# Kernel tuning notes

Measured on AMD Instinct MI355X. Metric: run time of the kernel, lower is better.

Reference implementation:

```python
import jax, jax.numpy as jnp
import numpy as np

S, N, V, E, H, L = 40, 256, 32000, 1024, 1024, 2


def _gru_step(x, h, wih, whh, bih, bhh):
    # PyTorch GRU cell, gate order [r, z, n]
    gi = x @ wih.T + bih          # (N, 3H)
    gh = h @ whh.T + bhh          # (N, 3H)
    ir, iz, inn = jnp.split(gi, 3, axis=-1)
    hr, hz, hn = jnp.split(gh, 3, axis=-1)
    r = jax.nn.sigmoid(ir + hr)
    z = jax.nn.sigmoid(iz + hz)
    n = jnp.tanh(inn + r * hn)
    return (1.0 - z) * n + z * h


def setup_inputs() -> dict:
    key = jax.random.key(0)
    ks = jax.random.split(key, 16)
    nrm = lambda k, shp: (jax.random.normal(k, shp, jnp.float32) * 0.05)
    return {
        "tokens": jax.random.randint(ks[0], (S, N), 0, V),
        "hidden": jnp.zeros((L, N, H), jnp.float32),
        "emb": nrm(ks[1], (V, E)),
        "enc_wih": nrm(ks[2], (L, 3 * H, E)),
        "enc_whh": nrm(ks[3], (L, 3 * H, H)),
        "enc_bih": nrm(ks[4], (L, 3 * H)),
        "enc_bhh": nrm(ks[5], (L, 3 * H)),
        "dec_wih": nrm(ks[6], (L, 3 * H, H)),
        "dec_whh": nrm(ks[7], (L, 3 * H, H)),
        "dec_bih": nrm(ks[8], (L, 3 * H)),
        "dec_bhh": nrm(ks[9], (L, 3 * H)),
        "attn_w": nrm(ks[10], (S, E + L * H)),
        "attn_b": nrm(ks[11], (S,)),
        "comb_w": nrm(ks[12], (H, 2 * H)),
        "comb_b": nrm(ks[13], (H,)),
    }


def reference(tokens, hidden, emb, enc_wih, enc_whh, enc_bih, enc_bhh,
              dec_wih, dec_whh, dec_bih, dec_bhh,
              attn_w, attn_b, comb_w, comb_b):
    x = emb[tokens]                      # (S, N, E) embedded input

    # ---- encoder: 2-layer GRU over the full sequence ----
    seq = x
    h_finals = []
    for l in range(L):
        wih, whh, bih, bhh = enc_wih[l], enc_whh[l], enc_bih[l], enc_bhh[l]
        def step(h, xt, wih=wih, whh=whh, bih=bih, bhh=bhh):
            h2 = _gru_step(xt, h, wih, whh, bih, bhh)
            return h2, h2
        hT, seq = jax.lax.scan(step, hidden[l], seq)
        h_finals.append(hT)
    h_n = jnp.stack(h_finals)            # (L, N, H)
    enc_out = jnp.swapaxes(seq, 0, 1)    # (N, S, H)

    # ---- attention decoder: scan over timesteps, carry decoder hidden ----
    def dec_step(h, emb_t):
        # h: (L, N, H), emb_t: (N, E)
        h_flat = jnp.swapaxes(h, 0, 1).reshape(N, L * H)
        logits = jnp.concatenate([emb_t, h_flat], axis=-1) @ attn_w.T + attn_b
        aw = jax.nn.softmax(logits, axis=-1)                   # (N, S)
        applied = jnp.einsum('ns,nsh->nh', aw, enc_out)        # (N, H)
        xcur = jax.nn.relu(
            jnp.concatenate([emb_t, applied], axis=-1) @ comb_w.T + comb_b)
        hs = []
        for l in range(L):
            hl = _gru_step(xcur, h[l], dec_wih[l], dec_whh[l],
                           dec_bih[l], dec_bhh[l])
            hs.append(hl)
            xcur = hl
        return jnp.stack(hs), xcur

    hT, outs = jax.lax.scan(dec_step, h_n, x)   # outs: (S, N, H)
    return outs, hT
```

## Files before the change

### kernel.cpp

```cpp
#include <hip/hip_runtime.h>
#include <hip/hip_bf16.h>

#define S_LEN 40
#define NB    256
#define EDIM  1024
#define HDIM  1024
#define NBLK  256
#define NTHR  768

typedef _Float16 f16;
typedef __attribute__((ext_vector_type(8))) _Float16 f16x8;
typedef __attribute__((ext_vector_type(4))) _Float16 f16x4;
typedef __attribute__((ext_vector_type(4))) float f32x4;

__device__ __forceinline__ float sigm(float x) {
    x = fminf(fmaxf(x, -30.f), 30.f);
    return 1.f / (1.f + __expf(-x));
}
__device__ __forceinline__ float tanh_fast(float x) {
    x = fminf(fmaxf(x, -15.f), 15.f);
    float e = __expf(2.f * x);
    return (e - 1.f) / (e + 1.f);
}

__device__ __forceinline__ void sysst_f16(f16* p, f16 v) {
    union { f16 f; unsigned short s; } u; u.f = v;
    unsigned int b = u.s;
    asm volatile("global_store_short %0, %1, off sc0 sc1" :: "v"(p), "v"(b) : "memory");
}

__device__ __forceinline__ void gbar1(unsigned* cnt, unsigned* gen) {
    asm volatile("s_waitcnt vmcnt(0)" ::: "memory");
    __syncthreads();
    if (threadIdx.x == 0) {
        unsigned g = __hip_atomic_load(gen, __ATOMIC_RELAXED, __HIP_MEMORY_SCOPE_AGENT);
        unsigned a = __hip_atomic_fetch_add(cnt, 1u, __ATOMIC_RELEASE, __HIP_MEMORY_SCOPE_AGENT);
        if (a == NBLK - 1) {
            __hip_atomic_store(cnt, 0u, __ATOMIC_RELAXED, __HIP_MEMORY_SCOPE_AGENT);
            __hip_atomic_fetch_add(gen, 1u, __ATOMIC_RELEASE, __HIP_MEMORY_SCOPE_AGENT);
        } else {
            while (__hip_atomic_load(gen, __ATOMIC_RELAXED, __HIP_MEMORY_SCOPE_AGENT) == g)
                __builtin_amdgcn_s_sleep(2);
        }
    }
    __syncthreads();
}

__device__ __forceinline__ void g2bar(unsigned* sync, unsigned xcd,
                                      unsigned M, unsigned NX) {
    asm volatile("s_waitcnt vmcnt(0)" ::: "memory");
    __syncthreads();
    if (threadIdx.x == 0) {
        unsigned* ggen = sync;
        unsigned* gcnt = sync + 1;
        unsigned* xa = sync + 16 + xcd * 16;
        unsigned g = __hip_atomic_load(ggen, __ATOMIC_RELAXED, __HIP_MEMORY_SCOPE_AGENT);
        unsigned a = __hip_atomic_fetch_add(xa, 1u, __ATOMIC_RELEASE, __HIP_MEMORY_SCOPE_AGENT);
        if (a == M - 1) {
            __hip_atomic_store(xa, 0u, __ATOMIC_RELAXED, __HIP_MEMORY_SCOPE_AGENT);
            unsigned b = __hip_atomic_fetch_add(gcnt, 1u, __ATOMIC_RELEASE, __HIP_MEMORY_SCOPE_AGENT);
            if (b == NX - 1) {
                __hip_atomic_store(gcnt, 0u, __ATOMIC_RELAXED, __HIP_MEMORY_SCOPE_AGENT);
                __hip_atomic_fetch_add(ggen, 1u, __ATOMIC_RELEASE, __HIP_MEMORY_SCOPE_AGENT);
            } else {
                while (__hip_atomic_load(ggen, __ATOMIC_RELAXED, __HIP_MEMORY_SCOPE_AGENT) == g)
                    __builtin_amdgcn_s_sleep(4);
            }
        } else {
            while (__hip_atomic_load(ggen, __ATOMIC_RELAXED, __HIP_MEMORY_SCOPE_AGENT) == g)
                __builtin_amdgcn_s_sleep(4);
        }
    }
    __syncthreads();
}

__global__ void k_init_sync(unsigned* s) {
    for (int k = threadIdx.x; k < 1024; k += 256) s[k] = 0;
}

__device__ __forceinline__ void probe_mn(int lane, int* mrow, int* ncol) {
    f16x8 pa, pb;
#pragma unroll
    for (int e = 0; e < 8; e++) {
        pa[e] = (f16)(float)(lane & 15);
        pb[e] = (f16)0.03125f;
    }
    f32x4 pacc = {0, 0, 0, 0};
    pacc = __builtin_amdgcn_mfma_f32_16x16x32_f16(pa, pb, pacc, 0, 0, 0);
#pragma unroll
    for (int r = 0; r < 4; r++) {
        int m = (int)(pacc[r] + 0.5f);
        int cg = ((lane >> 4) << 2) + r;
        mrow[r] = m;
        ncol[r] = (m == cg) ? (lane & 15) : cg;
    }
}

__global__ __launch_bounds__(256) void k_cvt4(const float* __restrict__ src,
                                              f16* __restrict__ dst, int n4) {
    int i = blockIdx.x * 256 + threadIdx.x;
    if (i < n4) {
        f32x4 v = ((const f32x4*)src)[i];
        f16x4 o = {(f16)v.x, (f16)v.y, (f16)v.z, (f16)v.w};
        ((f16x4*)dst)[i] = o;
    }
}
__global__ __launch_bounds__(256) void k_embed_cvt(const int* __restrict__ tok,
                                                   const float* __restrict__ emb,
                                                   f16* __restrict__ xe) {
    int b = blockIdx.x;
    int t = threadIdx.x;
    int token = tok[b];
    f32x4 v = ((const f32x4*)(emb + (size_t)token * EDIM))[t];
    f16x4 o = {(f16)v.x, (f16)v.y, (f16)v.z, (f16)v.w};
    ((f16x4*)(xe + (size_t)b * EDIM))[t] = o;
}

__device__ void gru_phase(
    char* lds, int cb, int rb, int tid, const int* mr, const int* nc,
    const f16* __restrict__ xsrc, const f16* __restrict__ hsrc,
    const f16* __restrict__ wih, const f16* __restrict__ whh,
    const float* __restrict__ bih, const float* __restrict__ bhh,
    f16* ho16, float* of_step, float* of_fin) {

    {
        constexpr int TOT = 8192;
        constexpr int IT = (TOT + NTHR - 1) / NTHR;
        f16x8 val[IT];
#pragma unroll
        for (int i = 0; i < IT; i++) {
            int c = tid + i * NTHR;
            if (c < TOT) {
                int isH = c >> 12;
                int cl = c & 4095;
                int row = cl >> 7, cc = cl & 127;
                const f16* src = (isH ? hsrc : xsrc) +
                                 (size_t)(rb + row) * 1024 + cc * 8;
                val[i] = *(const f16x8*)src;
            }
        }
#pragma unroll
        for (int i = 0; i < IT; i++) {
            int c = tid + i * NTHR;
            if (c < TOT) {
                int isH = c >> 12;
                int cl = c & 4095;
                int row = cl >> 7, cc = cl & 127;
                *(f16x8*)(lds + isH * 65536 + row * 2048 +
                          ((cc ^ (row & 7)) << 4)) = val[i];
            }
        }
    }
    __syncthreads();

    const int w = tid >> 6, lane = tid & 63;
    const int pair = w >> 1, kh = w & 1;
    const int gate = (pair >= 3) ? pair - 3 : pair;
    const int r0 = lane & 15, kk0 = (lane >> 4) * 8;
    const f16* B = ((pair < 3) ? wih : whh) + ((size_t)gate * HDIM + cb) * 1024;
    const f16* B0 = B + (size_t)r0 * 1024 + kk0 + kh * 512;
    const f16* B1 = B + (size_t)(r0 + 16) * 1024 + kk0 + kh * 512;
    const int abase = (pair < 3) ? 0 : 65536;
    const int swz = r0 & 7;
    const char* a0p = lds + abase + r0 * 2048;
    const char* a1p = lds + abase + (r0 + 16) * 2048;

    f32x4 acc00 = {0,0,0,0}, acc01 = {0,0,0,0}, acc10 = {0,0,0,0}, acc11 = {0,0,0,0};
#pragma unroll 4
    for (int k = 0; k < 512; k += 32) {
        int g = (kh * 512 + kk0 + k) >> 3;
        int off = (g ^ swz) << 4;
        f16x8 a0 = *(const f16x8*)(a0p + off);
        f16x8 a1 = *(const f16x8*)(a1p + off);
        f16x8 b0 = *(const f16x8*)(B0 + k);
        f16x8 b1 = *(const f16x8*)(B1 + k);
        acc00 = __builtin_amdgcn_mfma_f32_16x16x32_f16(a0, b0, acc00, 0, 0, 0);
        acc01 = __builtin_amdgcn_mfma_f32_16x16x32_f16(a0, b1, acc01, 0, 0, 0);
        acc10 = __builtin_amdgcn_mfma_f32_16x16x32_f16(a1, b0, acc10, 0, 0, 0);
        acc11 = __builtin_amdgcn_mfma_f32_16x16x32_f16(a1, b1, acc11, 0, 0, 0);
    }
    __syncthreads();

    float* red = (float*)lds;
    float* rw = red + w * 1024;
#pragma unroll
    for (int r = 0; r < 4; r++) {
        rw[mr[r] * 32 + nc[r]]             = acc00[r];
        rw[mr[r] * 32 + nc[r] + 16]        = acc01[r];
        rw[(mr[r] + 16) * 32 + nc[r]]      = acc10[r];
        rw[(mr[r] + 16) * 32 + nc[r] + 16] = acc11[r];
    }
    __syncthreads();

#pragma unroll
    for (int it = 0; it < 2; it++) {
        int i = tid + it * NTHR;
        if (i < 1024) {
            int rr = i >> 5, ccn = i & 31;
            int col = cb + ccn;
            int row = rb + rr;
            float gir = red[i]         + red[1024 + i];
            float giz = red[2048 + i]  + red[3072 + i];
            float gin = red[4096 + i]  + red[5120 + i];
            float ghr = red[6144 + i]  + red[7168 + i];
            float ghz = red[8192 + i]  + red[9216 + i];
            float ghn = red[10240 + i] + red[11264 + i];
            float r = sigm(gir + bih[col] + ghr + bhh[col]);
            float z = sigm(giz + bih[HDIM + col] + ghz + bhh[HDIM + col]);
            float n = tanh_fast(gin + bih[2 * HDIM + col] +
                                r * (ghn + bhh[2 * HDIM + col]));
            int gidx = col >> 3, within = col & 7;
            float hp = (float)*(const f16*)(lds + 65536 + rr * 2048 +
                                            ((gidx ^ (rr & 7)) << 4) + within * 2);
            float hn2 = (1.f - z) * n + z * hp;
            size_t idx = (size_t)row * HDIM + col;
            sysst_f16(ho16 + idx, (f16)hn2);
            if (of_step) of_step[idx] = hn2;
            if (of_fin)  of_fin[idx] = hn2;
        }
    }
}

__device__ void attn_phase(
    char* lds, int bid, int tid,
    const f16* __restrict__ xe_t, const f16* __restrict__ h0,
    const f16* __restrict__ h1,
    const f16* __restrict__ attn_w, const float* __restrict__ attn_b,
    const f16* __restrict__ enc16, f16* __restrict__ appl) {
    float* logit = (float*)(lds + 131072);
    float* awls  = logit + 64;
    const int n = bid;
    const int w = tid >> 6, lane = tid & 63;
    const size_t nrow = (size_t)n * 1024;

    {
        constexpr int TOT = 5504;
        constexpr int IT = (TOT + NTHR - 1) / NTHR;
        f16x8 val[IT];
#pragma unroll
        for (int i = 0; i < IT; i++) {
            int c = tid + i * NTHR;
            if (c < TOT) {
                if (c < 5120) {
                    int s = c >> 7, cc = c & 127;
                    val[i] = *(const f16x8*)(enc16 + ((size_t)s * NB + n) * 1024 + cc * 8);
                } else {
                    int r = c - 5120;
                    const f16* src = (r < 128) ? (xe_t + nrow + r * 8)
                                   : (r < 256) ? (h0 + nrow + (r - 128) * 8)
                                               : (h1 + nrow + (r - 256) * 8);
                    val[i] = *(const f16x8*)src;
                }
            }
        }
#pragma unroll
        for (int i = 0; i < IT; i++) {
            int c = tid + i * NTHR;
            if (c < TOT) {
                if (c < 5120) *(f16x8*)(lds + c * 16) = val[i];
                else          *(f16x8*)(lds + 81920 + (c - 5120) * 16) = val[i];
            }
        }
    }
    __syncthreads();

    if (w < 10) {
#pragma unroll
        for (int si = 0; si < 4; si++) {
            int s = w * 4 + si;
            const f16* wrow = attn_w + (size_t)s * 3072;
            float acc = 0.f;
#pragma unroll
            for (int jj = 0; jj < 6; jj++) {
                int j = lane + jj * 64;
                f16x8 a = *(const f16x8*)(lds + 81920 + j * 16);
                f16x8 b = *(const f16x8*)(wrow + j * 8);
#pragma unroll
                for (int e = 0; e < 8; e++)
                    acc = fmaf((float)a[e], (float)b[e], acc);
            }
            for (int o = 32; o; o >>= 1) acc += __shfl_down(acc, o);
            if (lane == 0) logit[s] = acc + attn_b[s];
        }
    }
    __syncthreads();

    if (w == 0) {
        float v = (lane < S_LEN) ? logit[lane] : -1e30f;
        float m = v;
        for (int o = 32; o; o >>= 1) m = fmaxf(m, __shfl_xor(m, o));
        float e = (lane < S_LEN) ? __expf(v - m) : 0.f;
        float sum = e;
        for (int o = 32; o; o >>= 1) sum += __shfl_xor(sum, o);
        if (lane < S_LEN) awls[lane] = e / sum;
    }
    __syncthreads();

    for (int col = tid; col < 1024; col += NTHR) {
        float acc = 0.f;
#pragma unroll
        for (int s = 0; s < S_LEN; s++)
            acc = fmaf(awls[s], (float)*(const f16*)(lds + s * 2048 + col * 2), acc);
        sysst_f16(appl + (size_t)n * 1024 + col, (f16)acc);
    }
}

__device__ void comb_phase(
    char* lds, int cb, int rb, int tid, const int* mr, const int* nc,
    const f16* __restrict__ xe_t, const f16* __restrict__ appl,
    const f16* __restrict__ Bw, const float* __restrict__ bias,
    f16* __restrict__ Cout) {

    {
        constexpr int TOT = 8192;
        constexpr int IT = (TOT + NTHR - 1) / NTHR;
        f16x8 val[IT];
#pragma unroll
        for (int i = 0; i < IT; i++) {
            int c = tid + i * NTHR;
            if (c < TOT) {
                int row = c >> 8, cc = c & 255;
                const f16* src = (cc < 128)
                    ? (xe_t + (size_t)(rb + row) * 1024 + cc * 8)
                    : (appl + (size_t)(rb + row) * 1024 + (cc - 128) * 8);
                val[i] = *(const f16x8*)src;
            }
        }
#pragma unroll
        for (int i = 0; i < IT; i++) {
            int c = tid + i * NTHR;
            if (c < TOT) {
                int row = c >> 8, cc = c & 255;
                *(f16x8*)(lds + row * 4096 + ((cc ^ (row & 7)) << 4)) = val[i];
            }
        }
    }
    __syncthreads();

    const int w = tid >> 6, lane = tid & 63;
    const int r0 = lane & 15, kk0 = (lane >> 4) * 8;
    const int c0 = (w * 64) / 12, c1 = ((w + 1) * 64) / 12;
    const f16* B0 = Bw + (size_t)(cb + r0) * 2048 + kk0;
    const f16* B1 = Bw + (size_t)(cb + r0 + 16) * 2048 + kk0;
    const int swz = r0 & 7;
    const char* a0p = lds + r0 * 4096;
    const char* a1p = lds + (r0 + 16) * 4096;

    f32x4 acc00 = {0,0,0,0}, acc01 = {0,0,0,0}, acc10 = {0,0,0,0}, acc11 = {0,0,0,0};
    for (int c = c0; c < c1; c++) {
        int g = (c * 32 + kk0) >> 3;
        int off = (g ^ swz) << 4;
        f16x8 a0 = *(const f16x8*)(a0p + off);
        f16x8 a1 = *(const f16x8*)(a1p + off);
        f16x8 b0 = *(const f16x8*)(B0 + c * 32);
        f16x8 b1 = *(const f16x8*)(B1 + c * 32);
        acc00 = __builtin_amdgcn_mfma_f32_16x16x32_f16(a0, b0, acc00, 0, 0, 0);
        acc01 = __builtin_amdgcn_mfma_f32_16x16x32_f16(a0, b1, acc01, 0, 0, 0);
        acc10 = __builtin_amdgcn_mfma_f32_16x16x32_f16(a1, b0, acc10, 0, 0, 0);
        acc11 = __builtin_amdgcn_mfma_f32_16x16x32_f16(a1, b1, acc11, 0, 0, 0);
    }
    __syncthreads();

    float* red = (float*)lds;
    float* rw = red + w * 1024;
#pragma unroll
    for (int r = 0; r < 4; r++) {
        rw[mr[r] * 32 + nc[r]]             = acc00[r];
        rw[mr[r] * 32 + nc[r] + 16]        = acc01[r];
        rw[(mr[r] + 16) * 32 + nc[r]]      = acc10[r];
        rw[(mr[r] + 16) * 32 + nc[r] + 16] = acc11[r];
    }
    __syncthreads();

#pragma unroll
    for (int it = 0; it < 2; it++) {
        int i = tid + it * NTHR;
        if (i < 1024) {
            float s = 0.f;
#pragma unroll
            for (int p = 0; p < 12; p++) s += red[p * 1024 + i];
            int rr = i >> 5, ccn = i & 31;
            s += bias[cb + ccn];
            s = fmaxf(s, 0.f);
            sysst_f16(Cout + (size_t)(rb + rr) * 1024 + cb + ccn, (f16)s);
        }
    }
}

__global__ __launch_bounds__(NTHR, 3) void k_mega(
    const f16* __restrict__ xe,
    f16* H0, f16* H1,
    const f16* __restrict__ w_eih, const f16* __restrict__ w_ehh,
    const float* __restrict__ enc_bih, const float* __restrict__ enc_bhh,
    const f16* __restrict__ w_dih, const f16* __restrict__ w_dhh,
    const float* __restrict__ dec_bih, const float* __restrict__ dec_bhh,
    const f16* __restrict__ w_attn, const float* __restrict__ attn_b,
    const f16* __restrict__ w_comb, const float* __restrict__ comb_b,
    f16* XC, f16* AP,
    float* out, unsigned* sync) {
    __shared__ char smem[131584];
    __shared__ unsigned s_meta[8];
    char* lds = smem;
    const int bid = blockIdx.x;
    const int tid = threadIdx.x;
    const int lane = tid & 63;
    const size_t NH = (size_t)NB * HDIM;

    int mr[4], nc[4];
    probe_mn(lane, mr, nc);

    if (tid == 0) {
        unsigned x;
        asm volatile("s_getreg_b32 %0, hwreg(20, 0, 32)" : "=s"(x));
        x &= 7;
        unsigned r = __hip_atomic_fetch_add(sync + 256 + x, 1u,
                                            __ATOMIC_RELAXED, __HIP_MEMORY_SCOPE_AGENT);
        s_meta[0] = x; s_meta[1] = r;
    }
    __syncthreads();
    gbar1(sync + 512, sync + 513);
    if (tid == 0) {
        unsigned M = __hip_atomic_load(sync + 256 + s_meta[0],
                                       __ATOMIC_RELAXED, __HIP_MEMORY_SCOPE_AGENT);
        unsigned nx = 0;
        bool uniform = true;
        for (int i = 0; i < 8; i++) {
            unsigned ci = __hip_atomic_load(sync + 256 + i, __ATOMIC_RELAXED,
                                            __HIP_MEMORY_SCOPE_AGENT);
            nx += (ci > 0) ? 1u : 0u;
            if (ci != 32) uniform = false;
        }
        s_meta[2] = M; s_meta[3] = nx;
        if (uniform) {
            s_meta[4] = (s_meta[0] * 4 + (s_meta[1] & 3)) * 32;
            s_meta[5] = (s_meta[1] >> 2) * 32;
        } else {
            s_meta[4] = (((unsigned)bid & 7) * 4 + (((unsigned)bid >> 3) & 3)) * 32;
            s_meta[5] = ((unsigned)bid >> 5) * 32;
        }
    }
    __syncthreads();
    const unsigned xcd = s_meta[0], M = s_meta[2], NX = s_meta[3];
    const int cb = (int)s_meta[4], rb = (int)s_meta[5];

    for (int t = 0; t < S_LEN; t++) {
        gru_phase(lds, cb, rb, tid, mr, nc,
                  xe + (size_t)t * NB * EDIM, H0 + (size_t)t * NH,
                  w_eih, w_ehh, enc_bih, enc_bhh,
                  H0 + (size_t)(t + 1) * NH, (float*)nullptr, (float*)nullptr);
        g2bar(sync, xcd, M, NX);
    }
    for (int t = 0; t < S_LEN; t++) {
        gru_phase(lds, cb, rb, tid, mr, nc,
                  H0 + (size_t)(t + 1) * NH, H1 + (size_t)t * NH,
                  w_eih + (size_t)3 * HDIM * EDIM, w_ehh + (size_t)3 * HDIM * HDIM,
                  enc_bih + 3 * HDIM, enc_bhh + 3 * HDIM,
                  H1 + (size_t)(t + 1) * NH, (float*)nullptr, (float*)nullptr);
        g2bar(sync, xcd, M, NX);
    }

    for (int t = 0; t < S_LEN; t++) {
        int g = S_LEN + t;
        attn_phase(lds, bid, tid,
                   xe + (size_t)t * NB * EDIM,
                   H0 + (size_t)g * NH, H1 + (size_t)g * NH,
                   w_attn, attn_b, H1 + NH, AP + (size_t)t * NH);
        g2bar(sync, xcd, M, NX);
        comb_phase(lds, cb, rb, tid, mr, nc,
                   xe + (size_t)t * NB * EDIM, AP + (size_t)t * NH,
                   w_comb, comb_b, XC + (size_t)t * NH);
        g2bar(sync, xcd, M, NX);
        gru_phase(lds, cb, rb, tid, mr, nc,
                  XC + (size_t)t * NH, H0 + (size_t)g * NH,
                  w_dih, w_dhh, dec_bih, dec_bhh,
                  H0 + (size_t)(g + 1) * NH, (float*)nullptr,
                  (t == S_LEN - 1) ? (out + (size_t)S_LEN * NH) : (float*)nullptr);
        g2bar(sync, xcd, M, NX);
        gru_phase(lds, cb, rb, tid, mr, nc,
                  H0 + (size_t)(g + 1) * NH, H1 + (size_t)g * NH,
                  w_dih + (size_t)3 * HDIM * HDIM, w_dhh + (size_t)3 * HDIM * HDIM,
                  dec_bih + 3 * HDIM, dec_bhh + 3 * HDIM,
                  H1 + (size_t)(g + 1) * NH, out + (size_t)t * NH,
                  (t == S_LEN - 1) ? (out + (size_t)(S_LEN + 1) * NH) : (float*)nullptr);
        g2bar(sync, xcd, M, NX);
    }
}

extern "C" void kernel_launch(void* const* d_in, const int* in_sizes, int n_in,
                              void* d_out, int out_size, void* d_ws, size_t ws_size,
                              hipStream_t stream) {
    const int*   tokens   = (const int*)d_in[0];
    const float* hidden   = (const float*)d_in[1];
    const float* emb      = (const float*)d_in[2];
    const float* enc_wih  = (const float*)d_in[3];
    const float* enc_whh  = (const float*)d_in[4];
    const float* enc_bih  = (const float*)d_in[5];
    const float* enc_bhh  = (const float*)d_in[6];
    const float* dec_wih  = (const float*)d_in[7];
    const float* dec_whh  = (const float*)d_in[8];
    const float* dec_bih  = (const float*)d_in[9];
    const float* dec_bhh  = (const float*)d_in[10];
    const float* attn_w   = (const float*)d_in[11];
    const float* attn_b   = (const float*)d_in[12];
    const float* comb_w   = (const float*)d_in[13];
    const float* comb_b   = (const float*)d_in[14];
    float* out = (float*)d_out;

    const size_t NH = (size_t)NB * HDIM;
    const size_t WSZ = (size_t)2 * 3 * HDIM * EDIM;

    f16* wp = (f16*)d_ws;
    f16 *w_eih = wp;  wp += WSZ;
    f16 *w_ehh = wp;  wp += WSZ;
    f16 *w_dih = wp;  wp += WSZ;
    f16 *w_dhh = wp;  wp += WSZ;
    f16 *w_comb = wp; wp += (size_t)HDIM * 2048;
    f16 *w_attn = wp; wp += (size_t)S_LEN * 3072;
    f16 *xe = wp;     wp += (size_t)S_LEN * NB * EDIM;
    f16 *H0 = wp;     wp += (size_t)(2 * S_LEN + 1) * NH;
    f16 *H1 = wp;     wp += (size_t)(2 * S_LEN + 1) * NH;
    f16 *XC = wp;     wp += (size_t)S_LEN * NH;
    f16 *AP = wp;     wp += (size_t)S_LEN * NH;
    unsigned* syncp = (unsigned*)((((uintptr_t)wp) + 255) & ~(uintptr_t)255);

    k_init_sync<<<1, 256, 0, stream>>>(syncp);

    k_cvt4<<<(int)(WSZ / 4 / 256), 256, 0, stream>>>(enc_wih, w_eih, (int)(WSZ / 4));
    k_cvt4<<<(int)(WSZ / 4 / 256), 256, 0, stream>>>(enc_whh, w_ehh, (int)(WSZ / 4));
    k_cvt4<<<(int)(WSZ / 4 / 256), 256, 0, stream>>>(dec_wih, w_dih, (int)(WSZ / 4));
    k_cvt4<<<(int)(WSZ / 4 / 256), 256, 0, stream>>>(dec_whh, w_dhh, (int)(WSZ / 4));
    k_cvt4<<<(int)(HDIM * 2048 / 4 / 256), 256, 0, stream>>>(comb_w, w_comb,
                                                             HDIM * 2048 / 4);
    k_cvt4<<<(S_LEN * 3072 / 4 + 255) / 256, 256, 0, stream>>>(attn_w, w_attn,
                                                               S_LEN * 3072 / 4);
    k_embed_cvt<<<S_LEN * NB, 256, 0, stream>>>(tokens, emb, xe);
    k_cvt4<<<(int)(NH / 4 / 256), 256, 0, stream>>>(hidden, H0, (int)(NH / 4));
    k_cvt4<<<(int)(NH / 4 / 256), 256, 0, stream>>>(hidden + NH, H1, (int)(NH / 4));

    k_mega<<<NBLK, NTHR, 0, stream>>>(
        xe, H0, H1,
        w_eih, w_ehh, enc_bih, enc_bhh,
        w_dih, w_dhh, dec_bih, dec_bhh,
        w_attn, attn_b, w_comb, comb_b,
        XC, AP, out, syncp);
}
```

Baseline: 5.441 ms.

## Read GEMM activations directly from global memory instead of staging through LDS

Removes the cooperative staging of activation tiles (x/h, comb inputs, encoder outputs) into swizzled LDS in the GRU, combine and attention phases. MFMA operands and the previous hidden value are now loaded straight from global/L2, and LDS is shrunk to just the reduction buffer and attention scratch. This cuts a staging pass and a barrier per phase and shrinks shared memory, at the cost of redundant, less coalesced global loads for the A operand. The A tile is now re-read from cache by each wave instead of once per block.

```diff
diff --git a/kernel.cpp b/kernel.cpp
--- a/kernel.cpp
+++ b/kernel.cpp
@@ -117,61 +117,29 @@
 }
 
 __device__ void gru_phase(
-    char* lds, int cb, int rb, int tid, const int* mr, const int* nc,
+    float* red, int cb, int rb, int tid, const int* mr, const int* nc,
     const f16* __restrict__ xsrc, const f16* __restrict__ hsrc,
     const f16* __restrict__ wih, const f16* __restrict__ whh,
     const float* __restrict__ bih, const float* __restrict__ bhh,
     f16* ho16, float* of_step, float* of_fin) {
 
-    {
-        constexpr int TOT = 8192;
-        constexpr int IT = (TOT + NTHR - 1) / NTHR;
-        f16x8 val[IT];
-#pragma unroll
-        for (int i = 0; i < IT; i++) {
-            int c = tid + i * NTHR;
-            if (c < TOT) {
-                int isH = c >> 12;
-                int cl = c & 4095;
-                int row = cl >> 7, cc = cl & 127;
-                const f16* src = (isH ? hsrc : xsrc) +
-                                 (size_t)(rb + row) * 1024 + cc * 8;
-                val[i] = *(const f16x8*)src;
-            }
-        }
-#pragma unroll
-        for (int i = 0; i < IT; i++) {
-            int c = tid + i * NTHR;
-            if (c < TOT) {
-                int isH = c >> 12;
-                int cl = c & 4095;
-                int row = cl >> 7, cc = cl & 127;
-                *(f16x8*)(lds + isH * 65536 + row * 2048 +
-                          ((cc ^ (row & 7)) << 4)) = val[i];
-            }
-        }
-    }
-    __syncthreads();
-
     const int w = tid >> 6, lane = tid & 63;
     const int pair = w >> 1, kh = w & 1;
     const int gate = (pair >= 3) ? pair - 3 : pair;
     const int r0 = lane & 15, kk0 = (lane >> 4) * 8;
+
+    const f16* A = (pair < 3) ? xsrc : hsrc;
+    const f16* A0 = A + (size_t)(rb + r0) * 1024 + kh * 512 + kk0;
+    const f16* A1 = A + (size_t)(rb + r0 + 16) * 1024 + kh * 512 + kk0;
     const f16* B = ((pair < 3) ? wih : whh) + ((size_t)gate * HDIM + cb) * 1024;
     const f16* B0 = B + (size_t)r0 * 1024 + kk0 + kh * 512;
     const f16* B1 = B + (size_t)(r0 + 16) * 1024 + kk0 + kh * 512;
-    const int abase = (pair < 3) ? 0 : 65536;
-    const int swz = r0 & 7;
-    const char* a0p = lds + abase + r0 * 2048;
-    const char* a1p = lds + abase + (r0 + 16) * 2048;
 
     f32x4 acc00 = {0,0,0,0}, acc01 = {0,0,0,0}, acc10 = {0,0,0,0}, acc11 = {0,0,0,0};
 #pragma unroll 4
     for (int k = 0; k < 512; k += 32) {
-        int g = (kh * 512 + kk0 + k) >> 3;
-        int off = (g ^ swz) << 4;
-        f16x8 a0 = *(const f16x8*)(a0p + off);
-        f16x8 a1 = *(const f16x8*)(a1p + off);
+        f16x8 a0 = *(const f16x8*)(A0 + k);
+        f16x8 a1 = *(const f16x8*)(A1 + k);
         f16x8 b0 = *(const f16x8*)(B0 + k);
         f16x8 b1 = *(const f16x8*)(B1 + k);
         acc00 = __builtin_amdgcn_mfma_f32_16x16x32_f16(a0, b0, acc00, 0, 0, 0);
@@ -179,9 +147,7 @@
         acc10 = __builtin_amdgcn_mfma_f32_16x16x32_f16(a1, b0, acc10, 0, 0, 0);
         acc11 = __builtin_amdgcn_mfma_f32_16x16x32_f16(a1, b1, acc11, 0, 0, 0);
     }
-    __syncthreads();
-
-    float* red = (float*)lds;
+
     float* rw = red + w * 1024;
 #pragma unroll
     for (int r = 0; r < 4; r++) {
@@ -209,9 +175,7 @@
             float z = sigm(giz + bih[HDIM + col] + ghz + bhh[HDIM + col]);
             float n = tanh_fast(gin + bih[2 * HDIM + col] +
                                 r * (ghn + bhh[2 * HDIM + col]));
-            int gidx = col >> 3, within = col & 7;
-            float hp = (float)*(const f16*)(lds + 65536 + rr * 2048 +
-                                            ((gidx ^ (rr & 7)) << 4) + within * 2);
+            float hp = (float)hsrc[(size_t)row * 1024 + col];
             float hn2 = (1.f - z) * n + z * hp;
             size_t idx = (size_t)row * HDIM + col;
             sysst_f16(ho16 + idx, (f16)hn2);
@@ -219,6 +183,7 @@
             if (of_fin)  of_fin[idx] = hn2;
         }
     }
+    __syncthreads();
 }
 
 __device__ void attn_phase(
@@ -227,40 +192,17 @@
     const f16* __restrict__ h1,
     const f16* __restrict__ attn_w, const float* __restrict__ attn_b,
     const f16* __restrict__ enc16, f16* __restrict__ appl) {
-    float* logit = (float*)(lds + 131072);
+    float* logit = (float*)(lds + 8192);
     float* awls  = logit + 64;
     const int n = bid;
     const int w = tid >> 6, lane = tid & 63;
     const size_t nrow = (size_t)n * 1024;
 
-    {
-        constexpr int TOT = 5504;
-        constexpr int IT = (TOT + NTHR - 1) / NTHR;
-        f16x8 val[IT];
-#pragma unroll
-        for (int i = 0; i < IT; i++) {
-            int c = tid + i * NTHR;
-            if (c < TOT) {
-                if (c < 5120) {
-                    int s = c >> 7, cc = c & 127;
-                    val[i] = *(const f16x8*)(enc16 + ((size_t)s * NB + n) * 1024 + cc * 8);
-                } else {
-                    int r = c - 5120;
-                    const f16* src = (r < 128) ? (xe_t + nrow + r * 8)
-                                   : (r < 256) ? (h0 + nrow + (r - 128) * 8)
-                                               : (h1 + nrow + (r - 256) * 8);
-                    val[i] = *(const f16x8*)src;
-                }
-            }
-        }
-#pragma unroll
-        for (int i = 0; i < IT; i++) {
-            int c = tid + i * NTHR;
-            if (c < TOT) {
-                if (c < 5120) *(f16x8*)(lds + c * 16) = val[i];
-                else          *(f16x8*)(lds + 81920 + (c - 5120) * 16) = val[i];
-            }
-        }
+    if (tid < 384) {
+        const f16* src = (tid < 128) ? (xe_t + nrow + tid * 8)
+                       : (tid < 256) ? (h0 + nrow + (tid - 128) * 8)
+                                     : (h1 + nrow + (tid - 256) * 8);
+        *(f16x8*)(lds + tid * 16) = *(const f16x8*)src;
     }
     __syncthreads();
 
@@ -273,7 +215,7 @@
 #pragma unroll
             for (int jj = 0; jj < 6; jj++) {
                 int j = lane + jj * 64;
-                f16x8 a = *(const f16x8*)(lds + 81920 + j * 16);
+                f16x8 a = *(const f16x8*)(lds + j * 16);
                 f16x8 b = *(const f16x8*)(wrow + j * 8);
 #pragma unroll
                 for (int e = 0; e < 8; e++)
@@ -300,58 +242,31 @@
         float acc = 0.f;
 #pragma unroll
         for (int s = 0; s < S_LEN; s++)
-            acc = fmaf(awls[s], (float)*(const f16*)(lds + s * 2048 + col * 2), acc);
-        sysst_f16(appl + (size_t)n * 1024 + col, (f16)acc);
-    }
+            acc = fmaf(awls[s], (float)enc16[(((size_t)s * NB + n) << 10) + col], acc);
+        sysst_f16(appl + nrow + col, (f16)acc);
+    }
+    __syncthreads();
 }
 
 __device__ void comb_phase(
-    char* lds, int cb, int rb, int tid, const int* mr, const int* nc,
+    float* red, int cb, int rb, int tid, const int* mr, const int* nc,
     const f16* __restrict__ xe_t, const f16* __restrict__ appl,
     const f16* __restrict__ Bw, const float* __restrict__ bias,
     f16* __restrict__ Cout) {
-
-    {
-        constexpr int TOT = 8192;
-        constexpr int IT = (TOT + NTHR - 1) / NTHR;
-        f16x8 val[IT];
-#pragma unroll
-        for (int i = 0; i < IT; i++) {
-            int c = tid + i * NTHR;
-            if (c < TOT) {
-                int row = c >> 8, cc = c & 255;
-                const f16* src = (cc < 128)
-                    ? (xe_t + (size_t)(rb + row) * 1024 + cc * 8)
-                    : (appl + (size_t)(rb + row) * 1024 + (cc - 128) * 8);
-                val[i] = *(const f16x8*)src;
-            }
-        }
-#pragma unroll
-        for (int i = 0; i < IT; i++) {
-            int c = tid + i * NTHR;
-            if (c < TOT) {
-                int row = c >> 8, cc = c & 255;
-                *(f16x8*)(lds + row * 4096 + ((cc ^ (row & 7)) << 4)) = val[i];
-            }
-        }
-    }
-    __syncthreads();
 
     const int w = tid >> 6, lane = tid & 63;
     const int r0 = lane & 15, kk0 = (lane >> 4) * 8;
     const int c0 = (w * 64) / 12, c1 = ((w + 1) * 64) / 12;
     const f16* B0 = Bw + (size_t)(cb + r0) * 2048 + kk0;
     const f16* B1 = Bw + (size_t)(cb + r0 + 16) * 2048 + kk0;
-    const int swz = r0 & 7;
-    const char* a0p = lds + r0 * 4096;
-    const char* a1p = lds + (r0 + 16) * 4096;
 
     f32x4 acc00 = {0,0,0,0}, acc01 = {0,0,0,0}, acc10 = {0,0,0,0}, acc11 = {0,0,0,0};
     for (int c = c0; c < c1; c++) {
-        int g = (c * 32 + kk0) >> 3;
-        int off = (g ^ swz) << 4;
-        f16x8 a0 = *(const f16x8*)(a0p + off);
-        f16x8 a1 = *(const f16x8*)(a1p + off);
+        int k = c * 32 + kk0;
+        const f16* Asel = (k < 1024) ? xe_t : appl;
+        int kk = (k < 1024) ? k : (k - 1024);
+        f16x8 a0 = *(const f16x8*)(Asel + (size_t)(rb + r0) * 1024 + kk);
+        f16x8 a1 = *(const f16x8*)(Asel + (size_t)(rb + r0 + 16) * 1024 + kk);
         f16x8 b0 = *(const f16x8*)(B0 + c * 32);
         f16x8 b1 = *(const f16x8*)(B1 + c * 32);
         acc00 = __builtin_amdgcn_mfma_f32_16x16x32_f16(a0, b0, acc00, 0, 0, 0);
@@ -359,9 +274,7 @@
         acc10 = __builtin_amdgcn_mfma_f32_16x16x32_f16(a1, b0, acc10, 0, 0, 0);
         acc11 = __builtin_amdgcn_mfma_f32_16x16x32_f16(a1, b1, acc11, 0, 0, 0);
     }
-    __syncthreads();
-
-    float* red = (float*)lds;
+
     float* rw = red + w * 1024;
 #pragma unroll
     for (int r = 0; r < 4; r++) {
@@ -385,6 +298,7 @@
             sysst_f16(Cout + (size_t)(rb + rr) * 1024 + cb + ccn, (f16)s);
         }
     }
+    __syncthreads();
 }
 
 __global__ __launch_bounds__(NTHR, 3) void k_mega(
@@ -398,9 +312,10 @@
     const f16* __restrict__ w_comb, const float* __restrict__ comb_b,
     f16* XC, f16* AP,
     float* out, unsigned* sync) {
-    __shared__ char smem[131584];
+    __shared__ char smem[49664];
     __shared__ unsigned s_meta[8];
     char* lds = smem;
+    float* red = (float*)smem;
     const int bid = blockIdx.x;
     const int tid = threadIdx.x;
     const int lane = tid & 63;
@@ -444,14 +359,14 @@
     const int cb = (int)s_meta[4], rb = (int)s_meta[5];
 
     for (int t = 0; t < S_LEN; t++) {
-        gru_phase(lds, cb, rb, tid, mr, nc,
+        gru_phase(red, cb, rb, tid, mr, nc,
                   xe + (size_t)t * NB * EDIM, H0 + (size_t)t * NH,
                   w_eih, w_ehh, enc_bih, enc_bhh,
                   H0 + (size_t)(t + 1) * NH, (float*)nullptr, (float*)nullptr);
         g2bar(sync, xcd, M, NX);
     }
     for (int t = 0; t < S_LEN; t++) {
-        gru_phase(lds, cb, rb, tid, mr, nc,
+        gru_phase(red, cb, rb, tid, mr, nc,
                   H0 + (size_t)(t + 1) * NH, H1 + (size_t)t * NH,
                   w_eih + (size_t)3 * HDIM * EDIM, w_ehh + (size_t)3 * HDIM * HDIM,
                   enc_bih + 3 * HDIM, enc_bhh + 3 * HDIM,
@@ -466,17 +381,17 @@
                    H0 + (size_t)g * NH, H1 + (size_t)g * NH,
                    w_attn, attn_b, H1 + NH, AP + (size_t)t * NH);
         g2bar(sync, xcd, M, NX);
-        comb_phase(lds, cb, rb, tid, mr, nc,
+        comb_phase(red, cb, rb, tid, mr, nc,
                    xe + (size_t)t * NB * EDIM, AP + (size_t)t * NH,
                    w_comb, comb_b, XC + (size_t)t * NH);
         g2bar(sync, xcd, M, NX);
-        gru_phase(lds, cb, rb, tid, mr, nc,
+        gru_phase(red, cb, rb, tid, mr, nc,
                   XC + (size_t)t * NH, H0 + (size_t)g * NH,
                   w_dih, w_dhh, dec_bih, dec_bhh,
                   H0 + (size_t)(g + 1) * NH, (float*)nullptr,
                   (t == S_LEN - 1) ? (out + (size_t)S_LEN * NH) : (float*)nullptr);
         g2bar(sync, xcd, M, NX);
-        gru_phase(lds, cb, rb, tid, mr, nc,
+        gru_phase(red, cb, rb, tid, mr, nc,
                   H0 + (size_t)(g + 1) * NH, H1 + (size_t)g * NH,
                   w_dih + (size_t)3 * HDIM * HDIM, w_dhh + (size_t)3 * HDIM * HDIM,
                   dec_bih + 3 * HDIM, dec_bhh + 3 * HDIM,
```

Result: slower. 6.615 ms (+21.6%).
